# Performance work log

Measured on AMD Instinct MI355X. Metric: run time of the kernel, lower is better.

The kernel has to match this reference:

```python
import jax, jax.numpy as jnp
import numpy as np

NUM_EMBEDDINGS = 1024
COMMITMENT_COST = 0.25


def setup_inputs() -> dict:
    key = jax.random.key(0)
    k1, k2 = jax.random.split(key)
    inputs = jax.random.normal(k1, (16, 64, 64, 64), dtype=jnp.float32)  # B,C,H,W with C=embedding_dim
    embedding = jax.random.normal(k2, (NUM_EMBEDDINGS, 64), dtype=jnp.float32)  # K,D codebook
    return {"inputs": inputs, "embedding": embedding}


def reference(inputs, embedding):
    # BCHW -> BHWC, flatten to (N, D)
    x = jnp.transpose(inputs, (0, 2, 3, 1))
    B, H, W, D = x.shape
    flat = x.reshape(-1, D)  # (N, D)

    distances = (jnp.sum(flat * flat, axis=1, keepdims=True)
                 + jnp.sum(embedding * embedding, axis=1)
                 - 2.0 * flat @ embedding.T)
    idx = jnp.argmin(distances, axis=1)           # (N,)
    indices = idx.reshape(B, H, W)
    encodings = jax.nn.one_hot(idx, NUM_EMBEDDINGS, dtype=flat.dtype)  # (N, K)

    # gather instead of one_hot @ embedding (same math, cheaper)
    quantized = embedding[idx].reshape(B, H, W, D)

    e_latent_loss = jnp.mean((jax.lax.stop_gradient(quantized) - x) ** 2)
    loss = COMMITMENT_COST * e_latent_loss

    # straight-through estimator
    q_ste = x + jax.lax.stop_gradient(quantized - x)

    avg_probs = jnp.mean(encodings, axis=0)
    perplexity = jnp.exp(-jnp.sum(avg_probs * jnp.log(avg_probs + 1e-10)))

    return loss, jnp.transpose(q_ste, (0, 3, 1, 2)), perplexity, encodings, indices
```

## Files before the change

kernel.cpp:

```cpp
#include <hip/hip_runtime.h>
#include <math.h>

#define NPTS 65536
#define DIM 64
#define NCODE 1024

typedef float f32x2 __attribute__((ext_vector_type(2)));
typedef float f32x4 __attribute__((ext_vector_type(4)));
typedef short bf16x8 __attribute__((ext_vector_type(8)));

#define OFF_LOSS 0ull
#define OFF_Q    1ull
#define OFF_PERP 4194305ull
#define OFF_ENC  4194306ull
#define OFF_IDX  71303170ull

__device__ __forceinline__ unsigned short bf16hi(float f) {
    unsigned u = __float_as_uint(f);
    unsigned r = u + 0x7FFFu + ((u >> 16) & 1u);
    return (unsigned short)(r >> 16);
}
__device__ __forceinline__ float bf16tof(unsigned short h) {
    return __uint_as_float(((unsigned)h) << 16);
}

__device__ __forceinline__ void cvt8(const float* p, bf16x8& hi, bf16x8& lo) {
    float4 a = *(const float4*)p;
    float4 b = *(const float4*)(p + 4);
    float v[8] = {a.x, a.y, a.z, a.w, b.x, b.y, b.z, b.w};
#pragma unroll
    for (int i = 0; i < 8; ++i) {
        unsigned short h = bf16hi(v[i]);
        hi[i] = (short)h;
        lo[i] = (short)bf16hi(v[i] - bf16tof(h));
    }
}
__device__ __forceinline__ void cvt8v(float4 a, float4 b, bf16x8& hi, bf16x8& lo) {
    float v[8] = {a.x, a.y, a.z, a.w, b.x, b.y, b.z, b.w};
#pragma unroll
    for (int i = 0; i < 8; ++i) {
        unsigned short h = bf16hi(v[i]);
        hi[i] = (short)h;
        lo[i] = (short)bf16hi(v[i] - bf16tof(h));
    }
}

__global__ __launch_bounds__(256, 3) void vq_fused(const float* __restrict__ in,
                                                   const float* __restrict__ emb,
                                                   float* __restrict__ out,
                                                   unsigned int* __restrict__ hist,
                                                   float* __restrict__ loss_acc) {
    __shared__ __align__(16) float lds_x[64][68];
    __shared__ unsigned long long cand[4][64];
    __shared__ int s_idx[64];

    const int tid  = threadIdx.x;
    const int lane = tid & 63;
    const int wv   = __builtin_amdgcn_readfirstlane(tid >> 6);

    const int P0 = blockIdx.x * 64;
    const int b  = P0 >> 12;
    const int h  = (P0 >> 6) & 63;
    const float* base = in + (size_t)b * (DIM * 4096) + h * 64;

    {
        int d  = tid >> 2;
        int wq = tid & 3;
        const float* rowp = base + (size_t)d * 4096 + wq * 16;
#pragma unroll
        for (int j = 0; j < 4; ++j) {
            float4 v = *(const float4*)(rowp + j * 4);
            int w0 = wq * 16 + j * 4;
            lds_x[w0 + 0][d] = v.x;
            lds_x[w0 + 1][d] = v.y;
            lds_x[w0 + 2][d] = v.z;
            lds_x[w0 + 3][d] = v.w;
        }
    }
    __syncthreads();

    const int m15 = lane & 15;
    const int g4  = lane >> 4;
    const int kb  = g4 * 8;
    const int c0w = wv * 256;

    bf16x8 Ahi[4][2], Alo[4][2];
#pragma unroll
    for (int pt = 0; pt < 4; ++pt) {
        int p = pt * 16 + m15;
        cvt8(&lds_x[p][kb],      Ahi[pt][0], Alo[pt][0]);
        cvt8(&lds_x[p][kb + 32], Ahi[pt][1], Alo[pt][1]);
    }

    float best[4][4];
    int   bestk[4][4];
#pragma unroll
    for (int pt = 0; pt < 4; ++pt)
#pragma unroll
        for (int r = 0; r < 4; ++r) { best[pt][r] = INFINITY; bestk[pt][r] = 0; }

    for (int ct = 0; ct < 16; ++ct) {
        const int code = c0w + ct * 16 + m15;
        const float* ep = emb + (size_t)code * DIM + kb;
        float4 e0 = *(const float4*)ep;
        float4 e1 = *(const float4*)(ep + 4);
        float4 e2a = *(const float4*)(ep + 32);
        float4 e3 = *(const float4*)(ep + 36);

        float sq = e0.x * e0.x;
        sq = fmaf(e0.y, e0.y, sq); sq = fmaf(e0.z, e0.z, sq); sq = fmaf(e0.w, e0.w, sq);
        sq = fmaf(e1.x, e1.x, sq); sq = fmaf(e1.y, e1.y, sq); sq = fmaf(e1.z, e1.z, sq); sq = fmaf(e1.w, e1.w, sq);
        sq = fmaf(e2a.x, e2a.x, sq); sq = fmaf(e2a.y, e2a.y, sq); sq = fmaf(e2a.z, e2a.z, sq); sq = fmaf(e2a.w, e2a.w, sq);
        sq = fmaf(e3.x, e3.x, sq); sq = fmaf(e3.y, e3.y, sq); sq = fmaf(e3.z, e3.z, sq); sq = fmaf(e3.w, e3.w, sq);
        sq += __shfl_xor(sq, 16, 64);
        sq += __shfl_xor(sq, 32, 64);
        const float e2v = sq;

        bf16x8 Bhi0, Blo0, Bhi1, Blo1;
        cvt8v(e0, e1, Bhi0, Blo0);
        cvt8v(e2a, e3, Bhi1, Blo1);

#pragma unroll
        for (int pt = 0; pt < 4; ++pt) {
            f32x4 acc = {0.f, 0.f, 0.f, 0.f};
            acc = __builtin_amdgcn_mfma_f32_16x16x32_bf16(Ahi[pt][0], Bhi0, acc, 0, 0, 0);
            acc = __builtin_amdgcn_mfma_f32_16x16x32_bf16(Ahi[pt][1], Bhi1, acc, 0, 0, 0);
            acc = __builtin_amdgcn_mfma_f32_16x16x32_bf16(Ahi[pt][0], Blo0, acc, 0, 0, 0);
            acc = __builtin_amdgcn_mfma_f32_16x16x32_bf16(Ahi[pt][1], Blo1, acc, 0, 0, 0);
            acc = __builtin_amdgcn_mfma_f32_16x16x32_bf16(Alo[pt][0], Bhi0, acc, 0, 0, 0);
            acc = __builtin_amdgcn_mfma_f32_16x16x32_bf16(Alo[pt][1], Bhi1, acc, 0, 0, 0);
#pragma unroll
            for (int r = 0; r < 4; ++r) {
                float dist = fmaf(-2.0f, acc[r], e2v);
                if (dist < best[pt][r]) { best[pt][r] = dist; bestk[pt][r] = code; }
            }
        }
    }

#pragma unroll
    for (int pt = 0; pt < 4; ++pt) {
#pragma unroll
        for (int r = 0; r < 4; ++r) {
            unsigned u = __float_as_uint(best[pt][r]);
            u = (u & 0x80000000u) ? ~u : (u | 0x80000000u);
            unsigned long long key = ((unsigned long long)u << 32) | (unsigned)bestk[pt][r];
#pragma unroll
            for (int sm = 1; sm < 16; sm <<= 1) {
                unsigned long long o = __shfl_xor(key, sm, 16);
                key = (o < key) ? o : key;
            }
            if (m15 == 0) cand[wv][pt * 16 + g4 * 4 + r] = key;
        }
    }
    __syncthreads();

    if (tid < 64) {
        unsigned long long k0 = cand[0][tid];
#pragma unroll
        for (int s = 1; s < 4; ++s) {
            unsigned long long o = cand[s][tid];
            if (o < k0) k0 = o;
        }
        int idx = (int)(k0 & 0xFFFFFFFFull);
        s_idx[tid] = idx;
        out[OFF_IDX + P0 + tid] = (float)idx;
        atomicAdd(&hist[idx], 1u);
    }
    __syncthreads();

    {
        const int w = lane;
        const int myidx = s_idx[w];
        const float* eq = emb + (size_t)myidx * DIM + wv * 16;
        float* qb = out + OFF_Q + ((size_t)b * 64 + wv * 16) * 4096 + h * 64 + w;
        float lsum = 0.f;
#pragma unroll
        for (int dd = 0; dd < 16; ++dd) {
            float x = lds_x[w][wv * 16 + dd];
            float diff = eq[dd] - x;
            lsum = fmaf(diff, diff, lsum);
            qb[(size_t)dd * 4096] = x + diff;
        }
        for (int off = 32; off > 0; off >>= 1) lsum += __shfl_down(lsum, off, 64);
        if (lane == 0) atomicAdd(loss_acc, lsum);
    }

    {
        f32x4* enc4 = (f32x4*)(out + OFF_ENC + (unsigned long long)P0 * NCODE);
#pragma unroll
        for (int rr = 0; rr < 16; ++rr) {
            const int row = wv * 16 + rr;
            const int target = s_idx[row];
#pragma unroll
            for (int k = 0; k < 4; ++k) {
                const int j = k * 64 + lane;
                const int c0 = j * 4;
                f32x4 v;
                v.x = (c0 + 0 == target) ? 1.0f : 0.0f;
                v.y = (c0 + 1 == target) ? 1.0f : 0.0f;
                v.z = (c0 + 2 == target) ? 1.0f : 0.0f;
                v.w = (c0 + 3 == target) ? 1.0f : 0.0f;
                __builtin_nontemporal_store(v, &enc4[(size_t)row * 256 + j]);
            }
        }
    }
}

__global__ __launch_bounds__(1024) void vq_finalize(const unsigned int* __restrict__ hist,
                                                    const float* __restrict__ loss_acc,
                                                    float* __restrict__ out) {
    int t = threadIdx.x;
    float c = (float)hist[t];
    float pv = c * (1.0f / (float)NPTS);
    float term = pv * logf(pv + 1e-10f);

    __shared__ float red[16];
    float s = term;
    for (int off = 32; off > 0; off >>= 1) s += __shfl_down(s, off, 64);
    if ((t & 63) == 0) red[t >> 6] = s;
    __syncthreads();
    if (t < 16) {
        float v = red[t];
        for (int off = 8; off > 0; off >>= 1) v += __shfl_down(v, off, 64);
        if (t == 0) {
            out[OFF_PERP] = expf(-v);
            out[OFF_LOSS] = 0.25f * loss_acc[0] * (1.0f / 4194304.0f);
        }
    }
}

extern "C" void kernel_launch(void* const* d_in, const int* in_sizes, int n_in,
                              void* d_out, int out_size, void* d_ws, size_t ws_size,
                              hipStream_t stream) {
    const float* in  = (const float*)d_in[0];
    const float* emb = (const float*)d_in[1];
    float* out = (float*)d_out;

    float* ws_f = (float*)d_ws;
    float* loss_acc = ws_f;
    unsigned int* hist = (unsigned int*)d_ws + 16;

    (void)hipMemsetAsync(d_ws, 0, (16 + NCODE) * sizeof(float), stream);

    vq_fused<<<NPTS / 64, 256, 0, stream>>>(in, emb, out, hist, loss_acc);
    vq_finalize<<<1, 1024, 0, stream>>>(hist, loss_acc, out);
}
```

Before: 105.4 us.

## Zero one-hot encodings early and prefetch codebook rows across tiles

The one-hot encodings tile is now zero-filled at kernel start with plain stores, so the stores can overlap the distance computation. Each point's single 1.0 is then written by one thread after the argmin. The codebook row loads are also software-pipelined, loading the next tile's embedding values one iteration ahead. Risks include ordering between the zero stores and the later one-hot store from another thread (same-address write ordering across waves is not guaranteed without a fence), and losing the nontemporal stores, which may pollute the cache.

New measurement: 109.0 us. 3.5% more time.

```diff
diff --git a/kernel.cpp b/kernel.cpp
--- a/kernel.cpp
+++ b/kernel.cpp
@@ -62,6 +62,7 @@
     const int b  = P0 >> 12;
     const int h  = (P0 >> 6) & 63;
     const float* base = in + (size_t)b * (DIM * 4096) + h * 64;
+    f32x4* enc4 = (f32x4*)(out + OFF_ENC + (unsigned long long)P0 * NCODE);
 
     {
         int d  = tid >> 2;
@@ -77,6 +78,17 @@
             lds_x[w0 + 3][d] = v.w;
         }
     }
+
+    {
+        const f32x4 z = {0.f, 0.f, 0.f, 0.f};
+#pragma unroll
+        for (int rr = 0; rr < 16; ++rr) {
+            const int row = wv * 16 + rr;
+#pragma unroll
+            for (int k = 0; k < 4; ++k)
+                enc4[(size_t)row * 256 + k * 64 + lane] = z;
+        }
+    }
     __syncthreads();
 
     const int m15 = lane & 15;
@@ -99,13 +111,26 @@
 #pragma unroll
         for (int r = 0; r < 4; ++r) { best[pt][r] = INFINITY; bestk[pt][r] = 0; }
 
+    float4 n0, n1, n2, n3;
+    {
+        const float* ep = emb + (size_t)(c0w + m15) * DIM + kb;
+        n0 = *(const float4*)ep;
+        n1 = *(const float4*)(ep + 4);
+        n2 = *(const float4*)(ep + 32);
+        n3 = *(const float4*)(ep + 36);
+    }
+
     for (int ct = 0; ct < 16; ++ct) {
-        const int code = c0w + ct * 16 + m15;
-        const float* ep = emb + (size_t)code * DIM + kb;
-        float4 e0 = *(const float4*)ep;
-        float4 e1 = *(const float4*)(ep + 4);
-        float4 e2a = *(const float4*)(ep + 32);
-        float4 e3 = *(const float4*)(ep + 36);
+        float4 e0 = n0, e1 = n1, e2a = n2, e3 = n3;
+
+        {
+            const int cnext = c0w + ((ct + 1) & 15) * 16 + m15;
+            const float* ep = emb + (size_t)cnext * DIM + kb;
+            n0 = *(const float4*)ep;
+            n1 = *(const float4*)(ep + 4);
+            n2 = *(const float4*)(ep + 32);
+            n3 = *(const float4*)(ep + 36);
+        }
 
         float sq = e0.x * e0.x;
         sq = fmaf(e0.y, e0.y, sq); sq = fmaf(e0.z, e0.z, sq); sq = fmaf(e0.w, e0.w, sq);
@@ -120,6 +145,7 @@
         cvt8v(e0, e1, Bhi0, Blo0);
         cvt8v(e2a, e3, Bhi1, Blo1);
 
+        const int code = c0w + ct * 16 + m15;
 #pragma unroll
         for (int pt = 0; pt < 4; ++pt) {
             f32x4 acc = {0.f, 0.f, 0.f, 0.f};
@@ -165,6 +191,15 @@
         s_idx[tid] = idx;
         out[OFF_IDX + P0 + tid] = (float)idx;
         atomicAdd(&hist[idx], 1u);
+
+        const int row = tid;
+        const int slot = idx & 3;
+        f32x4 v = {0.f, 0.f, 0.f, 0.f};
+        if (slot == 0) v.x = 1.0f;
+        else if (slot == 1) v.y = 1.0f;
+        else if (slot == 2) v.z = 1.0f;
+        else v.w = 1.0f;
+        enc4[(size_t)row * 256 + (idx >> 2)] = v;
     }
     __syncthreads();
 
@@ -183,26 +218,6 @@
         }
         for (int off = 32; off > 0; off >>= 1) lsum += __shfl_down(lsum, off, 64);
         if (lane == 0) atomicAdd(loss_acc, lsum);
-    }
-
-    {
-        f32x4* enc4 = (f32x4*)(out + OFF_ENC + (unsigned long long)P0 * NCODE);
-#pragma unroll
-        for (int rr = 0; rr < 16; ++rr) {
-            const int row = wv * 16 + rr;
-            const int target = s_idx[row];
-#pragma unroll
-            for (int k = 0; k < 4; ++k) {
-                const int j = k * 64 + lane;
-                const int c0 = j * 4;
-                f32x4 v;
-                v.x = (c0 + 0 == target) ? 1.0f : 0.0f;
-                v.y = (c0 + 1 == target) ? 1.0f : 0.0f;
-                v.z = (c0 + 2 == target) ? 1.0f : 0.0f;
-                v.w = (c0 + 3 == target) ? 1.0f : 0.0f;
-                __builtin_nontemporal_store(v, &enc4[(size_t)row * 256 + j]);
-            }
-        }
     }
 }
 
```

## Stage split-bf16 input in LDS and reload A fragments to raise occupancy

Applied to the files above, without the earlier changes.

The input tile is now converted to hi/lo bf16 once during the transpose and stored in two LDS arrays. The A operands are then reloaded from LDS inside the codebook loop instead of being held in registers. This frees registers so launch bounds can target four waves per SIMD instead of three. The quantized/loss epilogue moves after the one-hot stores and re-reads x from global memory, since the fp32 LDS copy is gone. In exchange the change adds LDS reads in the inner loop and a second global read of the inputs.

New measurement: 158.1 us. +50.0%, slower.

```diff
diff --git a/kernel.cpp b/kernel.cpp
--- a/kernel.cpp
+++ b/kernel.cpp
@@ -24,9 +24,7 @@
     return __uint_as_float(((unsigned)h) << 16);
 }
 
-__device__ __forceinline__ void cvt8(const float* p, bf16x8& hi, bf16x8& lo) {
-    float4 a = *(const float4*)p;
-    float4 b = *(const float4*)(p + 4);
+__device__ __forceinline__ void cvt8v(float4 a, float4 b, bf16x8& hi, bf16x8& lo) {
     float v[8] = {a.x, a.y, a.z, a.w, b.x, b.y, b.z, b.w};
 #pragma unroll
     for (int i = 0; i < 8; ++i) {
@@ -35,22 +33,14 @@
         lo[i] = (short)bf16hi(v[i] - bf16tof(h));
     }
 }
-__device__ __forceinline__ void cvt8v(float4 a, float4 b, bf16x8& hi, bf16x8& lo) {
-    float v[8] = {a.x, a.y, a.z, a.w, b.x, b.y, b.z, b.w};
-#pragma unroll
-    for (int i = 0; i < 8; ++i) {
-        unsigned short h = bf16hi(v[i]);
-        hi[i] = (short)h;
-        lo[i] = (short)bf16hi(v[i] - bf16tof(h));
-    }
-}
-
-__global__ __launch_bounds__(256, 3) void vq_fused(const float* __restrict__ in,
+
+__global__ __launch_bounds__(256, 4) void vq_fused(const float* __restrict__ in,
                                                    const float* __restrict__ emb,
                                                    float* __restrict__ out,
                                                    unsigned int* __restrict__ hist,
                                                    float* __restrict__ loss_acc) {
-    __shared__ __align__(16) float lds_x[64][68];
+    __shared__ __align__(16) unsigned short lds_hi[64][72];
+    __shared__ __align__(16) unsigned short lds_lo[64][72];
     __shared__ unsigned long long cand[4][64];
     __shared__ int s_idx[64];
 
@@ -70,11 +60,14 @@
 #pragma unroll
         for (int j = 0; j < 4; ++j) {
             float4 v = *(const float4*)(rowp + j * 4);
-            int w0 = wq * 16 + j * 4;
-            lds_x[w0 + 0][d] = v.x;
-            lds_x[w0 + 1][d] = v.y;
-            lds_x[w0 + 2][d] = v.z;
-            lds_x[w0 + 3][d] = v.w;
+            float vv[4] = {v.x, v.y, v.z, v.w};
+#pragma unroll
+            for (int i = 0; i < 4; ++i) {
+                int w0 = wq * 16 + j * 4 + i;
+                unsigned short hb = bf16hi(vv[i]);
+                lds_hi[w0][d] = hb;
+                lds_lo[w0][d] = bf16hi(vv[i] - bf16tof(hb));
+            }
         }
     }
     __syncthreads();
@@ -83,14 +76,6 @@
     const int g4  = lane >> 4;
     const int kb  = g4 * 8;
     const int c0w = wv * 256;
-
-    bf16x8 Ahi[4][2], Alo[4][2];
-#pragma unroll
-    for (int pt = 0; pt < 4; ++pt) {
-        int p = pt * 16 + m15;
-        cvt8(&lds_x[p][kb],      Ahi[pt][0], Alo[pt][0]);
-        cvt8(&lds_x[p][kb + 32], Ahi[pt][1], Alo[pt][1]);
-    }
 
     float best[4][4];
     int   bestk[4][4];
@@ -122,13 +107,18 @@
 
 #pragma unroll
         for (int pt = 0; pt < 4; ++pt) {
+            const int row = pt * 16 + m15;
+            bf16x8 ahi0 = *(const bf16x8*)&lds_hi[row][kb];
+            bf16x8 ahi1 = *(const bf16x8*)&lds_hi[row][kb + 32];
+            bf16x8 alo0 = *(const bf16x8*)&lds_lo[row][kb];
+            bf16x8 alo1 = *(const bf16x8*)&lds_lo[row][kb + 32];
             f32x4 acc = {0.f, 0.f, 0.f, 0.f};
-            acc = __builtin_amdgcn_mfma_f32_16x16x32_bf16(Ahi[pt][0], Bhi0, acc, 0, 0, 0);
-            acc = __builtin_amdgcn_mfma_f32_16x16x32_bf16(Ahi[pt][1], Bhi1, acc, 0, 0, 0);
-            acc = __builtin_amdgcn_mfma_f32_16x16x32_bf16(Ahi[pt][0], Blo0, acc, 0, 0, 0);
-            acc = __builtin_amdgcn_mfma_f32_16x16x32_bf16(Ahi[pt][1], Blo1, acc, 0, 0, 0);
-            acc = __builtin_amdgcn_mfma_f32_16x16x32_bf16(Alo[pt][0], Bhi0, acc, 0, 0, 0);
-            acc = __builtin_amdgcn_mfma_f32_16x16x32_bf16(Alo[pt][1], Bhi1, acc, 0, 0, 0);
+            acc = __builtin_amdgcn_mfma_f32_16x16x32_bf16(ahi0, Bhi0, acc, 0, 0, 0);
+            acc = __builtin_amdgcn_mfma_f32_16x16x32_bf16(ahi1, Bhi1, acc, 0, 0, 0);
+            acc = __builtin_amdgcn_mfma_f32_16x16x32_bf16(ahi0, Blo0, acc, 0, 0, 0);
+            acc = __builtin_amdgcn_mfma_f32_16x16x32_bf16(ahi1, Blo1, acc, 0, 0, 0);
+            acc = __builtin_amdgcn_mfma_f32_16x16x32_bf16(alo0, Bhi0, acc, 0, 0, 0);
+            acc = __builtin_amdgcn_mfma_f32_16x16x32_bf16(alo1, Bhi1, acc, 0, 0, 0);
 #pragma unroll
             for (int r = 0; r < 4; ++r) {
                 float dist = fmaf(-2.0f, acc[r], e2v);
@@ -167,23 +157,6 @@
         atomicAdd(&hist[idx], 1u);
     }
     __syncthreads();
-
-    {
-        const int w = lane;
-        const int myidx = s_idx[w];
-        const float* eq = emb + (size_t)myidx * DIM + wv * 16;
-        float* qb = out + OFF_Q + ((size_t)b * 64 + wv * 16) * 4096 + h * 64 + w;
-        float lsum = 0.f;
-#pragma unroll
-        for (int dd = 0; dd < 16; ++dd) {
-            float x = lds_x[w][wv * 16 + dd];
-            float diff = eq[dd] - x;
-            lsum = fmaf(diff, diff, lsum);
-            qb[(size_t)dd * 4096] = x + diff;
-        }
-        for (int off = 32; off > 0; off >>= 1) lsum += __shfl_down(lsum, off, 64);
-        if (lane == 0) atomicAdd(loss_acc, lsum);
-    }
 
     {
         f32x4* enc4 = (f32x4*)(out + OFF_ENC + (unsigned long long)P0 * NCODE);
@@ -204,6 +177,24 @@
             }
         }
     }
+
+    {
+        const int w = lane;
+        const int myidx = s_idx[w];
+        const float* eq = emb + (size_t)myidx * DIM + wv * 16;
+        const float* xb = in + ((size_t)b * 64 + wv * 16) * 4096 + h * 64 + w;
+        float* qb = out + OFF_Q + ((size_t)b * 64 + wv * 16) * 4096 + h * 64 + w;
+        float lsum = 0.f;
+#pragma unroll
+        for (int dd = 0; dd < 16; ++dd) {
+            float x = xb[(size_t)dd * 4096];
+            float diff = eq[dd] - x;
+            lsum = fmaf(diff, diff, lsum);
+            qb[(size_t)dd * 4096] = x + diff;
+        }
+        for (int off = 32; off > 0; off >>= 1) lsum += __shfl_down(lsum, off, 64);
+        if (lane == 0) atomicAdd(loss_acc, lsum);
+    }
 }
 
 __global__ __launch_bounds__(1024) void vq_finalize(const unsigned int* __restrict__ hist,
```

## Restructure VQ kernel to one wave per 16 points over full codebook

Applied to the files above, without the earlier changes.

Replaces the 256-thread block (64 points, codebook split across 4 waves, cross-wave LDS merge) with a single-wave block that handles 16 points against all 1024 codes. The cross-wave candidate reduction and one barrier go away, and each lane now holds far fewer A and accumulator registers. Independent MFMA chains are split into two accumulators to shorten dependency latency. The one-hot encoding stores switch from nontemporal to ordinary stores, and the dynamic LDS request is inflated, likely to cap blocks per CU. The cost is four times more codebook reads per point, since each 16-point wave reloads and reconverts the whole embedding table, plus 4096 small blocks.

Result: slower. 205.9 us (+95.4%).

```diff
diff --git a/kernel.cpp b/kernel.cpp
--- a/kernel.cpp
+++ b/kernel.cpp
@@ -5,7 +5,6 @@
 #define DIM 64
 #define NCODE 1024
 
-typedef float f32x2 __attribute__((ext_vector_type(2)));
 typedef float f32x4 __attribute__((ext_vector_type(4)));
 typedef short bf16x8 __attribute__((ext_vector_type(8)));
 
@@ -45,36 +44,30 @@
     }
 }
 
-__global__ __launch_bounds__(256, 3) void vq_fused(const float* __restrict__ in,
-                                                   const float* __restrict__ emb,
-                                                   float* __restrict__ out,
-                                                   unsigned int* __restrict__ hist,
-                                                   float* __restrict__ loss_acc) {
-    __shared__ __align__(16) float lds_x[64][68];
-    __shared__ unsigned long long cand[4][64];
-    __shared__ int s_idx[64];
-
-    const int tid  = threadIdx.x;
-    const int lane = tid & 63;
-    const int wv   = __builtin_amdgcn_readfirstlane(tid >> 6);
-
-    const int P0 = blockIdx.x * 64;
-    const int b  = P0 >> 12;
-    const int h  = (P0 >> 6) & 63;
-    const float* base = in + (size_t)b * (DIM * 4096) + h * 64;
+__global__ __launch_bounds__(64) void vq_wave(const float* __restrict__ in,
+                                              const float* __restrict__ emb,
+                                              float* __restrict__ out,
+                                              unsigned int* __restrict__ hist,
+                                              float* __restrict__ loss_acc) {
+    extern __shared__ float smem[];
+    float (*lds_x)[68] = (float (*)[68])smem;
+    int* lds_idx = (int*)(smem + 16 * 68);
+
+    const int lane = threadIdx.x;
+    const int P0   = blockIdx.x * 16;
+    const int b    = P0 >> 12;
+    const int h    = (P0 >> 6) & 63;
+    const int w0   = P0 & 63;
 
     {
-        int d  = tid >> 2;
-        int wq = tid & 3;
-        const float* rowp = base + (size_t)d * 4096 + wq * 16;
+        const float* rowp = in + (size_t)b * (DIM * 4096) + (size_t)lane * 4096 + h * 64 + w0;
 #pragma unroll
         for (int j = 0; j < 4; ++j) {
             float4 v = *(const float4*)(rowp + j * 4);
-            int w0 = wq * 16 + j * 4;
-            lds_x[w0 + 0][d] = v.x;
-            lds_x[w0 + 1][d] = v.y;
-            lds_x[w0 + 2][d] = v.z;
-            lds_x[w0 + 3][d] = v.w;
+            lds_x[j * 4 + 0][lane] = v.x;
+            lds_x[j * 4 + 1][lane] = v.y;
+            lds_x[j * 4 + 2][lane] = v.z;
+            lds_x[j * 4 + 3][lane] = v.w;
         }
     }
     __syncthreads();
@@ -82,25 +75,19 @@
     const int m15 = lane & 15;
     const int g4  = lane >> 4;
     const int kb  = g4 * 8;
-    const int c0w = wv * 256;
-
-    bf16x8 Ahi[4][2], Alo[4][2];
-#pragma unroll
-    for (int pt = 0; pt < 4; ++pt) {
-        int p = pt * 16 + m15;
-        cvt8(&lds_x[p][kb],      Ahi[pt][0], Alo[pt][0]);
-        cvt8(&lds_x[p][kb + 32], Ahi[pt][1], Alo[pt][1]);
-    }
-
-    float best[4][4];
-    int   bestk[4][4];
-#pragma unroll
-    for (int pt = 0; pt < 4; ++pt)
-#pragma unroll
-        for (int r = 0; r < 4; ++r) { best[pt][r] = INFINITY; bestk[pt][r] = 0; }
-
-    for (int ct = 0; ct < 16; ++ct) {
-        const int code = c0w + ct * 16 + m15;
+
+    bf16x8 Ahi0, Ahi1, Alo0, Alo1;
+    cvt8(&lds_x[m15][kb],      Ahi0, Alo0);
+    cvt8(&lds_x[m15][kb + 32], Ahi1, Alo1);
+
+    float best[4];
+    int   bestk[4];
+#pragma unroll
+    for (int r = 0; r < 4; ++r) { best[r] = INFINITY; bestk[r] = 0; }
+
+#pragma unroll 4
+    for (int ct = 0; ct < 64; ++ct) {
+        const int code = ct * 16 + m15;
         const float* ep = emb + (size_t)code * DIM + kb;
         float4 e0 = *(const float4*)ep;
         float4 e1 = *(const float4*)(ep + 4);
@@ -120,63 +107,49 @@
         cvt8v(e0, e1, Bhi0, Blo0);
         cvt8v(e2a, e3, Bhi1, Blo1);
 
-#pragma unroll
-        for (int pt = 0; pt < 4; ++pt) {
-            f32x4 acc = {0.f, 0.f, 0.f, 0.f};
-            acc = __builtin_amdgcn_mfma_f32_16x16x32_bf16(Ahi[pt][0], Bhi0, acc, 0, 0, 0);
-            acc = __builtin_amdgcn_mfma_f32_16x16x32_bf16(Ahi[pt][1], Bhi1, acc, 0, 0, 0);
-            acc = __builtin_amdgcn_mfma_f32_16x16x32_bf16(Ahi[pt][0], Blo0, acc, 0, 0, 0);
-            acc = __builtin_amdgcn_mfma_f32_16x16x32_bf16(Ahi[pt][1], Blo1, acc, 0, 0, 0);
-            acc = __builtin_amdgcn_mfma_f32_16x16x32_bf16(Alo[pt][0], Bhi0, acc, 0, 0, 0);
-            acc = __builtin_amdgcn_mfma_f32_16x16x32_bf16(Alo[pt][1], Bhi1, acc, 0, 0, 0);
-#pragma unroll
-            for (int r = 0; r < 4; ++r) {
-                float dist = fmaf(-2.0f, acc[r], e2v);
-                if (dist < best[pt][r]) { best[pt][r] = dist; bestk[pt][r] = code; }
-            }
-        }
-    }
-
-#pragma unroll
-    for (int pt = 0; pt < 4; ++pt) {
+        f32x4 aa = {0.f, 0.f, 0.f, 0.f};
+        f32x4 ab = {0.f, 0.f, 0.f, 0.f};
+        aa = __builtin_amdgcn_mfma_f32_16x16x32_bf16(Ahi0, Bhi0, aa, 0, 0, 0);
+        ab = __builtin_amdgcn_mfma_f32_16x16x32_bf16(Ahi1, Bhi1, ab, 0, 0, 0);
+        aa = __builtin_amdgcn_mfma_f32_16x16x32_bf16(Ahi0, Blo0, aa, 0, 0, 0);
+        ab = __builtin_amdgcn_mfma_f32_16x16x32_bf16(Ahi1, Blo1, ab, 0, 0, 0);
+        aa = __builtin_amdgcn_mfma_f32_16x16x32_bf16(Alo0, Bhi0, aa, 0, 0, 0);
+        ab = __builtin_amdgcn_mfma_f32_16x16x32_bf16(Alo1, Bhi1, ab, 0, 0, 0);
 #pragma unroll
         for (int r = 0; r < 4; ++r) {
-            unsigned u = __float_as_uint(best[pt][r]);
-            u = (u & 0x80000000u) ? ~u : (u | 0x80000000u);
-            unsigned long long key = ((unsigned long long)u << 32) | (unsigned)bestk[pt][r];
-#pragma unroll
-            for (int sm = 1; sm < 16; sm <<= 1) {
-                unsigned long long o = __shfl_xor(key, sm, 16);
-                key = (o < key) ? o : key;
-            }
-            if (m15 == 0) cand[wv][pt * 16 + g4 * 4 + r] = key;
+            float dist = fmaf(-2.0f, aa[r] + ab[r], e2v);
+            if (dist < best[r]) { best[r] = dist; bestk[r] = code; }
+        }
+    }
+
+#pragma unroll
+    for (int r = 0; r < 4; ++r) {
+        unsigned u = __float_as_uint(best[r]);
+        u = (u & 0x80000000u) ? ~u : (u | 0x80000000u);
+        unsigned long long key = ((unsigned long long)u << 32) | (unsigned)bestk[r];
+#pragma unroll
+        for (int sm = 1; sm < 16; sm <<= 1) {
+            unsigned long long o = __shfl_xor(key, sm, 16);
+            key = (o < key) ? o : key;
+        }
+        if (m15 == 0) {
+            const int pt  = g4 * 4 + r;
+            const int idx = (int)(key & 0xFFFFFFFFull);
+            lds_idx[pt] = idx;
+            out[OFF_IDX + P0 + pt] = (float)idx;
+            atomicAdd(&hist[idx], 1u);
         }
     }
     __syncthreads();
 
-    if (tid < 64) {
-        unsigned long long k0 = cand[0][tid];
-#pragma unroll
-        for (int s = 1; s < 4; ++s) {
-            unsigned long long o = cand[s][tid];
-            if (o < k0) k0 = o;
-        }
-        int idx = (int)(k0 & 0xFFFFFFFFull);
-        s_idx[tid] = idx;
-        out[OFF_IDX + P0 + tid] = (float)idx;
-        atomicAdd(&hist[idx], 1u);
-    }
-    __syncthreads();
-
     {
-        const int w = lane;
-        const int myidx = s_idx[w];
-        const float* eq = emb + (size_t)myidx * DIM + wv * 16;
-        float* qb = out + OFF_Q + ((size_t)b * 64 + wv * 16) * 4096 + h * 64 + w;
+        const int myidx = lds_idx[m15];
+        const float* eq = emb + (size_t)myidx * DIM + g4 * 16;
+        float* qb = out + OFF_Q + ((size_t)b * 64 + g4 * 16) * 4096 + h * 64 + w0 + m15;
         float lsum = 0.f;
 #pragma unroll
         for (int dd = 0; dd < 16; ++dd) {
-            float x = lds_x[w][wv * 16 + dd];
+            float x = lds_x[m15][g4 * 16 + dd];
             float diff = eq[dd] - x;
             lsum = fmaf(diff, diff, lsum);
             qb[(size_t)dd * 4096] = x + diff;
@@ -189,8 +162,7 @@
         f32x4* enc4 = (f32x4*)(out + OFF_ENC + (unsigned long long)P0 * NCODE);
 #pragma unroll
         for (int rr = 0; rr < 16; ++rr) {
-            const int row = wv * 16 + rr;
-            const int target = s_idx[row];
+            const int target = lds_idx[rr];
 #pragma unroll
             for (int k = 0; k < 4; ++k) {
                 const int j = k * 64 + lane;
@@ -200,7 +172,7 @@
                 v.y = (c0 + 1 == target) ? 1.0f : 0.0f;
                 v.z = (c0 + 2 == target) ? 1.0f : 0.0f;
                 v.w = (c0 + 3 == target) ? 1.0f : 0.0f;
-                __builtin_nontemporal_store(v, &enc4[(size_t)row * 256 + j]);
+                enc4[(size_t)rr * 256 + j] = v;
             }
         }
     }
@@ -242,6 +214,6 @@
 
     (void)hipMemsetAsync(d_ws, 0, (16 + NCODE) * sizeof(float), stream);
 
-    vq_fused<<<NPTS / 64, 256, 0, stream>>>(in, emb, out, hist, loss_acc);
+    vq_wave<<<NPTS / 16, 64, 19456, stream>>>(in, emb, out, hist, loss_acc);
     vq_finalize<<<1, 1024, 0, stream>>>(hist, loss_acc, out);
 }
```
